# Kernel tuning notes

Measured on AMD Instinct MI355X. Metric: run time of the kernel, lower is better.

The kernel has to match this reference:

```python
import jax, jax.numpy as jnp
import numpy as np

N_NODES = 100000
N_EDGES = 3200000
IN_FEATS = 128
HIDDEN = 64
N_CLASSES = 16


def gcn_conv(x, src, dst, W, b, num_nodes):
    """PyG GCNConv (default settings): add self-loops, symmetric norm,
    linear transform, scatter-sum aggregation at dst, then bias."""
    # degree counts include self-loops (fill value 1.0)
    deg = jnp.zeros((num_nodes,), x.dtype).at[dst].add(1.0) + 1.0
    dinv = jax.lax.rsqrt(deg)  # deg >= 1, no inf handling needed
    h = x @ W  # [N, out]
    # edge messages: norm(src,dst) * h[src], aggregated at dst
    norm = dinv[src] * dinv[dst]  # [E]
    msg = h[src] * norm[:, None]  # [E, out]
    out = jax.ops.segment_sum(msg, dst, num_segments=num_nodes)
    # self-loop contribution: norm = dinv[i]^2
    out = out + h * (dinv * dinv)[:, None]
    return out + b


def setup_inputs() -> dict:
    key = jax.random.key(0)
    k1, k2, k3, k4 = jax.random.split(key, 4)
    x = jax.random.normal(k1, (N_NODES, IN_FEATS), dtype=jnp.float32)
    edge_index = jax.random.randint(k2, (2, N_EDGES), 0, N_NODES, dtype=jnp.int64)
    W1 = jax.random.normal(k3, (IN_FEATS, HIDDEN), dtype=jnp.float32) * (1.0 / np.sqrt(IN_FEATS))
    b1 = jnp.zeros((HIDDEN,), jnp.float32)
    W2 = jax.random.normal(k4, (HIDDEN, N_CLASSES), dtype=jnp.float32) * (1.0 / np.sqrt(HIDDEN))
    b2 = jnp.zeros((N_CLASSES,), jnp.float32)
    return {"x": x, "edge_index": edge_index, "W1": W1, "b1": b1, "W2": W2, "b2": b2}


def reference(x, edge_index, W1, b1, W2, b2):
    src, dst = edge_index[0], edge_index[1]
    h = gcn_conv(x, src, dst, W1, b1, N_NODES)
    h = jax.nn.relu(h)  # dropout is identity in eval mode
    out = gcn_conv(h, src, dst, W2, b2, N_NODES)
    return out
```

## Files before the change

### kernel.cpp

```cpp
#include <hip/hip_runtime.h>
#include <hip/hip_fp16.h>
#include <stdint.h>

#define N_NODES   100000
#define N_HALF    50000
#define N_EDGES   3200000
#define F_IN      128
#define F_HID     64
#define F_OUT     16

typedef _Float16 h2v __attribute__((ext_vector_type(2)));
typedef _Float16 h4v __attribute__((ext_vector_type(4)));

#define BSHIFT    8
#define NBUCK     391
#define NBLK_P    800
#define CHUNK_E   (N_EDGES / NBLK_P)
#define PSTRIDE   9856

#define G1_TM     128
#define G1_BLOCKS ((N_NODES + G1_TM - 1) / G1_TM)
#define XS_LD     132

#define OFF_RS       0
#define OFF_LEN      400000
#define OFF_DINV     800000
#define OFF_GCNT     1200000
#define OFF_CSR      1201616
#define OFF_HS1      8909008
#define OFF_OUT1A    21709008
#define OFF_OUT1B    34509008
#define OFF_HS2      47309008
#define OFF_PAIRS    OFF_OUT1A

__global__ __launch_bounds__(256, 4) void k_partition(const void* __restrict__ ei,
                                                      int* __restrict__ gcnt,
                                                      unsigned* __restrict__ pairs) {
    __shared__ unsigned long long st[CHUNK_E];
    __shared__ int h[NBUCK];
    __shared__ int cur[NBUCK];
    __shared__ int is64s;
    int t = threadIdx.x;
    if (t < 64) {
        const unsigned* u = (const unsigned*)ei;
        unsigned lo = u[2 * t], hi = u[2 * t + 1];
        int bad = (hi != 0u || lo >= 100000u) ? 1 : 0;
        unsigned long long mask = __ballot(bad);
        if (t == 0) is64s = (mask == 0ull);
    }
    for (int i = t; i < NBUCK; i += 256) h[i] = 0;
    __syncthreads();
    int shift = 2 + is64s;
    const char* sp = (const char*)ei;
    const char* dp = sp + ((size_t)N_EDGES << shift);
#define LDS_IDX(p, e) (*(const unsigned*)((p) + ((size_t)(e) << shift)))
    int base = blockIdx.x * CHUNK_E;
    int i = t;
    for (; i + 768 < CHUNK_E; i += 1024) {
        int e0 = base + i, e1 = e0 + 256, e2 = e0 + 512, e3 = e0 + 768;
        unsigned s0 = LDS_IDX(sp, e0), s1 = LDS_IDX(sp, e1);
        unsigned s2 = LDS_IDX(sp, e2), s3 = LDS_IDX(sp, e3);
        unsigned d0 = LDS_IDX(dp, e0), d1 = LDS_IDX(dp, e1);
        unsigned d2 = LDS_IDX(dp, e2), d3 = LDS_IDX(dp, e3);
        st[i]       = ((unsigned long long)s0 << 32) | d0;
        st[i + 256] = ((unsigned long long)s1 << 32) | d1;
        st[i + 512] = ((unsigned long long)s2 << 32) | d2;
        st[i + 768] = ((unsigned long long)s3 << 32) | d3;
        atomicAdd(&h[d0 >> BSHIFT], 1);
        atomicAdd(&h[d1 >> BSHIFT], 1);
        atomicAdd(&h[d2 >> BSHIFT], 1);
        atomicAdd(&h[d3 >> BSHIFT], 1);
    }
    for (; i < CHUNK_E; i += 256) {
        unsigned s = LDS_IDX(sp, base + i);
        unsigned d = LDS_IDX(dp, base + i);
        st[i] = ((unsigned long long)s << 32) | d;
        atomicAdd(&h[d >> BSHIFT], 1);
    }
#undef LDS_IDX
    __syncthreads();
    for (int j = t; j < NBUCK; j += 256) {
        int c = h[j];
        cur[j] = c ? atomicAdd(&gcnt[j], c) : 0;
    }
    __syncthreads();
    i = t;
    for (; i + 768 < CHUNK_E; i += 1024) {
        unsigned long long v0 = st[i],       v1 = st[i + 256];
        unsigned long long v2 = st[i + 512], v3 = st[i + 768];
        unsigned d0 = (unsigned)v0, d1 = (unsigned)v1;
        unsigned d2 = (unsigned)v2, d3 = (unsigned)v3;
        int p0 = atomicAdd(&cur[d0 >> BSHIFT], 1);
        int p1 = atomicAdd(&cur[d1 >> BSHIFT], 1);
        int p2 = atomicAdd(&cur[d2 >> BSHIFT], 1);
        int p3 = atomicAdd(&cur[d3 >> BSHIFT], 1);
        if (p0 < PSTRIDE) pairs[(d0 >> BSHIFT) * PSTRIDE + p0] = ((unsigned)(v0 >> 32) << 8) | (d0 & 255u);
        if (p1 < PSTRIDE) pairs[(d1 >> BSHIFT) * PSTRIDE + p1] = ((unsigned)(v1 >> 32) << 8) | (d1 & 255u);
        if (p2 < PSTRIDE) pairs[(d2 >> BSHIFT) * PSTRIDE + p2] = ((unsigned)(v2 >> 32) << 8) | (d2 & 255u);
        if (p3 < PSTRIDE) pairs[(d3 >> BSHIFT) * PSTRIDE + p3] = ((unsigned)(v3 >> 32) << 8) | (d3 & 255u);
    }
    for (; i < CHUNK_E; i += 256) {
        unsigned long long v = st[i];
        unsigned d = (unsigned)v;
        int b = d >> BSHIFT;
        int p = atomicAdd(&cur[b], 1);
        if (p < PSTRIDE)
            pairs[b * PSTRIDE + p] = ((unsigned)(v >> 32) << 8) | (d & 255u);
    }
}

__global__ __launch_bounds__(512) void k_build(const unsigned* __restrict__ pairs,
                                               const int* __restrict__ gcnt,
                                               int* __restrict__ rowstart,
                                               int* __restrict__ lens,
                                               float* __restrict__ dinv,
                                               unsigned short* __restrict__ csr) {
    __shared__ unsigned prS[PSTRIDE];
    __shared__ unsigned short csrS[PSTRIDE];
    __shared__ int c0S[256], c1S[256], scanS[256], pos0[256], pos1[256];
    __shared__ int totpadS;
    int b = blockIdx.x, t = threadIdx.x;
    if (t < 256) { c0S[t] = 0; c1S[t] = 0; }
    __syncthreads();
    int tot = gcnt[b]; if (tot > PSTRIDE) tot = PSTRIDE;
    int base = b * PSTRIDE;
    for (int i = t; i < tot; i += 512) {
        unsigned pr = pairs[base + i];
        prS[i] = pr;
        if ((pr >> 8) < (unsigned)N_HALF) atomicAdd(&c0S[pr & 255u], 1);
        else                              atomicAdd(&c1S[pr & 255u], 1);
    }
    __syncthreads();
    int tpad = 0, p0a = 0;
    if (t < 256) {
        p0a = (c0S[t] + 3) & ~3;
        tpad = p0a + ((c1S[t] + 3) & ~3);
        scanS[t] = tpad;
    }
    __syncthreads();
    for (int off = 1; off < 256; off <<= 1) {
        int add = 0;
        if (t < 256 && t >= off) add = scanS[t - off];
        __syncthreads();
        if (t < 256) scanS[t] += add;
        __syncthreads();
    }
    if (t < 256) {
        int rs = scanS[t] - tpad;
        pos0[t] = rs;
        pos1[t] = rs + p0a;
        int d = (b << BSHIFT) + t;
        if (d < N_NODES) {
            rowstart[d] = base + rs;
            lens[d] = c0S[t] | (c1S[t] << 16);
            dinv[d] = rsqrtf((float)(c0S[t] + c1S[t]) + 1.0f);
        }
        if (t == 255) totpadS = scanS[255];
    }
    __syncthreads();
    for (int i = t; i < tot; i += 512) {
        unsigned pr = prS[i];
        unsigned s = pr >> 8;
        int d = pr & 255u;
        if (s < (unsigned)N_HALF) {
            int p = atomicAdd(&pos0[d], 1);
            csrS[p] = (unsigned short)s;
        } else {
            int p = atomicAdd(&pos1[d], 1);
            csrS[p] = (unsigned short)(s - N_HALF);
        }
    }
    __syncthreads();
    int nchunk = (totpadS + 7) >> 3;
    uint4* dst = (uint4*)(csr + base);
    const uint4* srcp = (const uint4*)csrS;
    for (int i = t; i < nchunk; i += 512) dst[i] = srcp[i];
}

__global__ __launch_bounds__(256) void k_gemm1(const float* __restrict__ x,
                                               const float* __restrict__ W1,
                                               const float* __restrict__ dinv,
                                               __half* __restrict__ hs1) {
    __shared__ float xsT[64 * XS_LD];
    __shared__ float ws[64 * 64];
    int t = threadIdx.x;
    int nblock = blockIdx.x * G1_TM;
    int ng = t >> 4, og = t & 15;
    int n0 = ng * 8;
    float acc[8][4] = {};

    int snode = nblock + (t >> 1);
    int koff = (t & 1) * 32;
    int nl = t >> 1;

    for (int chunk = 0; chunk < 2; ++chunk) {
        int kbase = chunk * 64;
        {
            float4 v[8];
            if (snode < N_NODES) {
                const float4* src = (const float4*)(x + (size_t)snode * F_IN + kbase + koff);
#pragma unroll
                for (int c = 0; c < 8; ++c) v[c] = src[c];
            } else {
#pragma unroll
                for (int c = 0; c < 8; ++c) v[c] = make_float4(0.f, 0.f, 0.f, 0.f);
            }
#pragma unroll
            for (int c = 0; c < 8; ++c) {
                int k = koff + c * 4;
                xsT[(k + 0) * XS_LD + nl] = v[c].x;
                xsT[(k + 1) * XS_LD + nl] = v[c].y;
                xsT[(k + 2) * XS_LD + nl] = v[c].z;
                xsT[(k + 3) * XS_LD + nl] = v[c].w;
            }
        }
        {
            const float4* wsrc = (const float4*)(W1 + kbase * F_HID);
            float4* wdst = (float4*)ws;
#pragma unroll
            for (int c = 0; c < 4; ++c) wdst[c * 256 + t] = wsrc[c * 256 + t];
        }
        __syncthreads();

#pragma unroll 4
        for (int k = 0; k < 64; ++k) {
            const float4* xr = (const float4*)(xsT + k * XS_LD + n0);
            float4 a0 = xr[0], a1 = xr[1];
            float4 bv = *(const float4*)(ws + k * 64 + og * 4);
            float a[8] = {a0.x, a0.y, a0.z, a0.w, a1.x, a1.y, a1.z, a1.w};
            float bb[4] = {bv.x, bv.y, bv.z, bv.w};
#pragma unroll
            for (int i = 0; i < 8; ++i)
#pragma unroll
                for (int j = 0; j < 4; ++j)
                    acc[i][j] += a[i] * bb[j];
        }
        __syncthreads();
    }

#pragma unroll
    for (int i = 0; i < 8; ++i) {
        int node = nblock + n0 + i;
        if (node < N_NODES) {
            float dv = dinv[node];
            union { __half2 h[2]; float2 f; } u;
            u.h[0] = __floats2half2_rn(acc[i][0] * dv, acc[i][1] * dv);
            u.h[1] = __floats2half2_rn(acc[i][2] * dv, acc[i][3] * dv);
            *(float2*)(hs1 + ((size_t)(og >> 3) * N_NODES + node) * 32 + (og & 7) * 4) = u.f;
        }
    }
}

__global__ __launch_bounds__(256) void k_agg1(const __half* __restrict__ hs1,
                                              const unsigned short* __restrict__ csr,
                                              const int* __restrict__ rowstart,
                                              const int* __restrict__ lens,
                                              __half* __restrict__ out1a,
                                              __half* __restrict__ out1b) {
    int bid = blockIdx.x;
    int combo = bid & 3;
    int chunk = combo & 1, half = combo >> 1;
    int nb = bid >> 2;
    int w = threadIdx.x >> 6, lane = threadIdx.x & 63;
    int slot = lane >> 3, fp = lane & 7;
    int n = nb * 32 + w * 8 + slot;
    const char* T = (const char*)hs1
                  + (size_t)chunk * ((size_t)N_NODES * 64)
                  + (size_t)half * ((size_t)N_HALF * 64);
    unsigned fo = fp * 8u;
    int rs = rowstart[n];
    int L = lens[n];
    int c0 = L & 0xffff;
    int start = half ? (rs + ((c0 + 3) & ~3)) : rs;
    int c = half ? (L >> 16) : c0;
    h4v a0 = {(_Float16)0.f, (_Float16)0.f, (_Float16)0.f, (_Float16)0.f};
    h4v a1 = a0, a2 = a0, a3 = a0;
    const unsigned long long* Q = (const unsigned long long*)csr;
    int q0 = start >> 2;
    int nq = c >> 2;
#define ROW1(idx) (*(const h4v*)(T + (unsigned)(idx) * 64u + fo))
    int q = 0;
    unsigned long long ea = 0ull, eb = 0ull;
    if (q + 2 <= nq) { ea = Q[q0]; eb = Q[q0 + 1]; }
    while (q + 2 <= nq) {
        unsigned long long ca = ea, cb = eb;
        q += 2;
        if (q + 2 <= nq) { ea = Q[q0 + q]; eb = Q[q0 + q + 1]; }
        h4v t0 = ROW1(ca & 0xffffu);
        h4v t1 = ROW1((ca >> 16) & 0xffffu);
        h4v t2 = ROW1((ca >> 32) & 0xffffu);
        h4v t3 = ROW1(ca >> 48);
        h4v t4 = ROW1(cb & 0xffffu);
        h4v t5 = ROW1((cb >> 16) & 0xffffu);
        h4v t6 = ROW1((cb >> 32) & 0xffffu);
        h4v t7 = ROW1(cb >> 48);
        a0 += t0; a1 += t1; a2 += t2; a3 += t3;
        a0 += t4; a1 += t5; a2 += t6; a3 += t7;
    }
    if (q < nq) {
        unsigned long long e = Q[q0 + q];
        a0 += ROW1(e & 0xffffu);
        a1 += ROW1((e >> 16) & 0xffffu);
        a2 += ROW1((e >> 32) & 0xffffu);
        a3 += ROW1(e >> 48);
    }
    for (int j = start + (nq << 2); j < start + c; ++j)
        a0 += ROW1(csr[j]);
    if ((n >= N_HALF) == (half != 0))
        a1 += ROW1(n - half * N_HALF);
#undef ROW1
    float s0 = ((float)a0[0] + (float)a1[0]) + ((float)a2[0] + (float)a3[0]);
    float s1 = ((float)a0[1] + (float)a1[1]) + ((float)a2[1] + (float)a3[1]);
    float s2 = ((float)a0[2] + (float)a1[2]) + ((float)a2[2] + (float)a3[2]);
    float s3 = ((float)a0[3] + (float)a1[3]) + ((float)a2[3] + (float)a3[3]);
    union { __half2 h[2]; float2 f; } u;
    u.h[0] = __floats2half2_rn(s0, s1);
    u.h[1] = __floats2half2_rn(s2, s3);
    __half* dst = (half ? out1b : out1a) + (size_t)n * F_HID + chunk * 32 + fp * 4;
    *(float2*)dst = u.f;
}

__global__ __launch_bounds__(256) void k_gemm2(const __half* __restrict__ out1a,
                                               const __half* __restrict__ out1b,
                                               const float* __restrict__ W2,
                                               const float* __restrict__ dinv,
                                               const float* __restrict__ b1,
                                               __half* __restrict__ hs2) {
    __shared__ float ws[F_HID * F_OUT];
    __shared__ float b1s[F_HID];
    int t = threadIdx.x;
    ((float4*)ws)[t] = ((const float4*)W2)[t];
    if (t < 16) ((float4*)b1s)[t] = ((const float4*)b1)[t];
    __syncthreads();
    int tid = blockIdx.x * 256 + t;
    int n = tid >> 2;
    if (n >= N_NODES) return;
    int cq = (tid & 3) << 2;
    float dv = dinv[n];
    const h2v* A = (const h2v*)(out1a + (size_t)n * F_HID);
    const h2v* B = (const h2v*)(out1b + (size_t)n * F_HID);
    float4 acc = make_float4(0.f, 0.f, 0.f, 0.f);
#pragma unroll 4
    for (int k4 = 0; k4 < 16; ++k4) {
        h2v pa0 = A[k4 * 2], pa1 = A[k4 * 2 + 1];
        h2v pb0 = B[k4 * 2], pb1 = B[k4 * 2 + 1];
        float h0 = fmaxf(dv * ((float)pa0.x + (float)pb0.x) + b1s[k4 * 4 + 0], 0.f);
        float h1 = fmaxf(dv * ((float)pa0.y + (float)pb0.y) + b1s[k4 * 4 + 1], 0.f);
        float h2 = fmaxf(dv * ((float)pa1.x + (float)pb1.x) + b1s[k4 * 4 + 2], 0.f);
        float h3 = fmaxf(dv * ((float)pa1.y + (float)pb1.y) + b1s[k4 * 4 + 3], 0.f);
        float4 w0 = *(const float4*)(ws + (k4 * 4 + 0) * F_OUT + cq);
        float4 w1 = *(const float4*)(ws + (k4 * 4 + 1) * F_OUT + cq);
        float4 w2 = *(const float4*)(ws + (k4 * 4 + 2) * F_OUT + cq);
        float4 w3 = *(const float4*)(ws + (k4 * 4 + 3) * F_OUT + cq);
        acc.x += h0 * w0.x + h1 * w1.x + h2 * w2.x + h3 * w3.x;
        acc.y += h0 * w0.y + h1 * w1.y + h2 * w2.y + h3 * w3.y;
        acc.z += h0 * w0.z + h1 * w1.z + h2 * w2.z + h3 * w3.z;
        acc.w += h0 * w0.w + h1 * w1.w + h2 * w2.w + h3 * w3.w;
    }
    union { __half2 h2x[2]; float2 f; } u;
    u.h2x[0] = __floats2half2_rn(acc.x * dv, acc.y * dv);
    u.h2x[1] = __floats2half2_rn(acc.z * dv, acc.w * dv);
    *(float2*)(hs2 + (size_t)n * F_OUT + cq) = u.f;
}

__global__ __launch_bounds__(128) void k_agg2(const __half* __restrict__ hs2,
                                              const unsigned short* __restrict__ csr,
                                              const int* __restrict__ rowstart,
                                              const int* __restrict__ lens,
                                              const float* __restrict__ dinv,
                                              const float* __restrict__ b2,
                                              float* __restrict__ out) {
    int w = threadIdx.x >> 6, lane = threadIdx.x & 63;
    int slot = lane >> 2, fp = lane & 3;
    int n = blockIdx.x * 32 + w * 16 + slot;
    unsigned fo = fp * 8u;
    int rs = rowstart[n];
    int L = lens[n];
    int c0 = L & 0xffff, c1 = L >> 16;
    const unsigned long long* Q = (const unsigned long long*)csr;
    h4v a0 = {(_Float16)0.f, (_Float16)0.f, (_Float16)0.f, (_Float16)0.f};
    h4v a1 = a0, a2 = a0, a3 = a0;
#pragma unroll
    for (int half = 0; half < 2; ++half) {
        const char* T = (const char*)hs2 + (size_t)half * ((size_t)N_HALF * 32);
        int start = half ? (rs + ((c0 + 3) & ~3)) : rs;
        int c = half ? c1 : c0;
        int q0 = start >> 2;
        int nq = c >> 2;
#define ROW2(idx) (*(const h4v*)(T + (unsigned)(idx) * 32u + fo))
        int q = 0;
        unsigned long long ea = 0ull, eb = 0ull;
        if (q + 2 <= nq) { ea = Q[q0]; eb = Q[q0 + 1]; }
        while (q + 2 <= nq) {
            unsigned long long ca = ea, cb = eb;
            q += 2;
            if (q + 2 <= nq) { ea = Q[q0 + q]; eb = Q[q0 + q + 1]; }
            h4v t0 = ROW2(ca & 0xffffu);
            h4v t1 = ROW2((ca >> 16) & 0xffffu);
            h4v t2 = ROW2((ca >> 32) & 0xffffu);
            h4v t3 = ROW2(ca >> 48);
            h4v t4 = ROW2(cb & 0xffffu);
            h4v t5 = ROW2((cb >> 16) & 0xffffu);
            h4v t6 = ROW2((cb >> 32) & 0xffffu);
            h4v t7 = ROW2(cb >> 48);
            a0 += t0; a1 += t1; a2 += t2; a3 += t3;
            a0 += t4; a1 += t5; a2 += t6; a3 += t7;
        }
        if (q < nq) {
            unsigned long long e = Q[q0 + q];
            a0 += ROW2(e & 0xffffu);
            a1 += ROW2((e >> 16) & 0xffffu);
            a2 += ROW2((e >> 32) & 0xffffu);
            a3 += ROW2(e >> 48);
        }
        for (int j = start + (nq << 2); j < start + c; ++j)
            a0 += ROW2(csr[j]);
#undef ROW2
    }
    a1 += *(const h4v*)((const char*)hs2 + (unsigned)n * 32u + fo);
    float dv = dinv[n];
    int fb = fp * 4;
    float s0 = ((float)a0[0] + (float)a1[0]) + ((float)a2[0] + (float)a3[0]);
    float s1 = ((float)a0[1] + (float)a1[1]) + ((float)a2[1] + (float)a3[1]);
    float s2 = ((float)a0[2] + (float)a1[2]) + ((float)a2[2] + (float)a3[2]);
    float s3 = ((float)a0[3] + (float)a1[3]) + ((float)a2[3] + (float)a3[3]);
    float ox0 = dv * s0 + b2[fb + 0];
    float ox1 = dv * s1 + b2[fb + 1];
    float ox2 = dv * s2 + b2[fb + 2];
    float ox3 = dv * s3 + b2[fb + 3];
    float4* dst = (float4*)(out + (size_t)n * F_OUT + fb);
    *dst = make_float4(ox0, ox1, ox2, ox3);
}

extern "C" void kernel_launch(void* const* d_in, const int* in_sizes, int n_in,
                              void* d_out, int out_size, void* d_ws, size_t ws_size,
                              hipStream_t stream) {
    const float* x  = (const float*)d_in[0];
    const void*  ei = d_in[1];
    const float* W1 = (const float*)d_in[2];
    const float* b1 = (const float*)d_in[3];
    const float* W2 = (const float*)d_in[4];
    const float* b2 = (const float*)d_in[5];
    float* out = (float*)d_out;

    char* ws = (char*)d_ws;
    int*            rowstart = (int*)(ws + OFF_RS);
    int*            lens     = (int*)(ws + OFF_LEN);
    float*          dinv     = (float*)(ws + OFF_DINV);
    int*            gcnt     = (int*)(ws + OFF_GCNT);
    unsigned short* csr      = (unsigned short*)(ws + OFF_CSR);
    __half*         hs1      = (__half*)(ws + OFF_HS1);
    __half*         out1a    = (__half*)(ws + OFF_OUT1A);
    __half*         out1b    = (__half*)(ws + OFF_OUT1B);
    __half*         hs2      = (__half*)(ws + OFF_HS2);
    unsigned*       pairs    = (unsigned*)(ws + OFF_PAIRS);

    (void)hipMemsetAsync(gcnt, 0, NBUCK * sizeof(int), stream);
    k_partition<<<NBLK_P, 256, 0, stream>>>(ei, gcnt, pairs);
    k_build    <<<NBUCK, 512, 0, stream>>>(pairs, gcnt, rowstart, lens, dinv, csr);

    k_gemm1<<<G1_BLOCKS, 256, 0, stream>>>(x, W1, dinv, hs1);
    k_agg1 <<<12500, 256, 0, stream>>>(hs1, csr, rowstart, lens, out1a, out1b);
    k_gemm2<<<(N_NODES * 4 + 255) / 256, 256, 0, stream>>>(out1a, out1b, W2, dinv, b1, hs2);
    k_agg2 <<<3125, 128, 0, stream>>>(hs2, csr, rowstart, lens, dinv, b2, out);
}
```

Measured before the change: 281.4 us.

## Use nontemporal loads for streamed inputs and split agg1 into per-chunk launches

Streaming reads of edge indices, partition pairs and x in the gemm are switched to nontemporal loads so they do not evict reusable data from cache. The first aggregation kernel is split into two launches, one per 32-feature chunk of hs1, instead of interleaving both chunks across blocks in one launch. This shrinks the gather working set per launch (half the hs1 table) to improve L2 hit rate, at the cost of an extra launch and re-reading CSR indices twice serially.

Result: slower. 293.7 us (+4.4%).

```diff
diff --git a/kernel.cpp b/kernel.cpp
--- a/kernel.cpp
+++ b/kernel.cpp
@@ -11,6 +11,7 @@
 
 typedef _Float16 h2v __attribute__((ext_vector_type(2)));
 typedef _Float16 h4v __attribute__((ext_vector_type(4)));
+typedef float    f4v __attribute__((ext_vector_type(4)));
 
 #define BSHIFT    8
 #define NBUCK     391
@@ -53,7 +54,7 @@
     int shift = 2 + is64s;
     const char* sp = (const char*)ei;
     const char* dp = sp + ((size_t)N_EDGES << shift);
-#define LDS_IDX(p, e) (*(const unsigned*)((p) + ((size_t)(e) << shift)))
+#define LDS_IDX(p, e) __builtin_nontemporal_load((const unsigned*)((p) + ((size_t)(e) << shift)))
     int base = blockIdx.x * CHUNK_E;
     int i = t;
     for (; i + 768 < CHUNK_E; i += 1024) {
@@ -125,7 +126,7 @@
     int tot = gcnt[b]; if (tot > PSTRIDE) tot = PSTRIDE;
     int base = b * PSTRIDE;
     for (int i = t; i < tot; i += 512) {
-        unsigned pr = pairs[base + i];
+        unsigned pr = __builtin_nontemporal_load(pairs + base + i);
         prS[i] = pr;
         if ((pr >> 8) < (unsigned)N_HALF) atomicAdd(&c0S[pr & 255u], 1);
         else                              atomicAdd(&c1S[pr & 255u], 1);
@@ -196,22 +197,22 @@
     for (int chunk = 0; chunk < 2; ++chunk) {
         int kbase = chunk * 64;
         {
-            float4 v[8];
+            f4v v[8];
             if (snode < N_NODES) {
-                const float4* src = (const float4*)(x + (size_t)snode * F_IN + kbase + koff);
-#pragma unroll
-                for (int c = 0; c < 8; ++c) v[c] = src[c];
+                const f4v* src = (const f4v*)(x + (size_t)snode * F_IN + kbase + koff);
+#pragma unroll
+                for (int c = 0; c < 8; ++c) v[c] = __builtin_nontemporal_load(src + c);
             } else {
 #pragma unroll
-                for (int c = 0; c < 8; ++c) v[c] = make_float4(0.f, 0.f, 0.f, 0.f);
+                for (int c = 0; c < 8; ++c) v[c] = (f4v){0.f, 0.f, 0.f, 0.f};
             }
 #pragma unroll
             for (int c = 0; c < 8; ++c) {
                 int k = koff + c * 4;
-                xsT[(k + 0) * XS_LD + nl] = v[c].x;
-                xsT[(k + 1) * XS_LD + nl] = v[c].y;
-                xsT[(k + 2) * XS_LD + nl] = v[c].z;
-                xsT[(k + 3) * XS_LD + nl] = v[c].w;
+                xsT[(k + 0) * XS_LD + nl] = v[c][0];
+                xsT[(k + 1) * XS_LD + nl] = v[c][1];
+                xsT[(k + 2) * XS_LD + nl] = v[c][2];
+                xsT[(k + 3) * XS_LD + nl] = v[c][3];
             }
         }
         {
@@ -256,11 +257,11 @@
                                               const int* __restrict__ rowstart,
                                               const int* __restrict__ lens,
                                               __half* __restrict__ out1a,
-                                              __half* __restrict__ out1b) {
+                                              __half* __restrict__ out1b,
+                                              int chunk) {
     int bid = blockIdx.x;
-    int combo = bid & 3;
-    int chunk = combo & 1, half = combo >> 1;
-    int nb = bid >> 2;
+    int half = bid & 1;
+    int nb = bid >> 1;
     int w = threadIdx.x >> 6, lane = threadIdx.x & 63;
     int slot = lane >> 3, fp = lane & 7;
     int n = nb * 32 + w * 8 + slot;
@@ -460,7 +461,8 @@
     k_build    <<<NBUCK, 512, 0, stream>>>(pairs, gcnt, rowstart, lens, dinv, csr);
 
     k_gemm1<<<G1_BLOCKS, 256, 0, stream>>>(x, W1, dinv, hs1);
-    k_agg1 <<<12500, 256, 0, stream>>>(hs1, csr, rowstart, lens, out1a, out1b);
+    k_agg1 <<<6250, 256, 0, stream>>>(hs1, csr, rowstart, lens, out1a, out1b, 0);
+    k_agg1 <<<6250, 256, 0, stream>>>(hs1, csr, rowstart, lens, out1a, out1b, 1);
     k_gemm2<<<(N_NODES * 4 + 255) / 256, 256, 0, stream>>>(out1a, out1b, W2, dinv, b1, hs2);
     k_agg2 <<<3125, 128, 0, stream>>>(hs2, csr, rowstart, lens, dinv, b2, out);
 }
```

## Shrink gemm1 tiles for occupancy and use nontemporal loads for streamed inputs

Applied to the files above, without the earlier changes.

Halves the gemm1 node tile to 64 and the K chunk to 32, cuts per-thread accumulators from 8x4 to 4x4, and adds launch bounds requesting 4 blocks per CU. The aim is less LDS and fewer registers per block, so more blocks stay resident to hide the latency of streaming x. Edge-index, pairs and x reads now use nontemporal loads so these single-use streams do not evict cached data. In exchange W1 is reloaded per smaller block and there are more barrier rounds.

Result: no change. 282.9 us (+0.5%).

```diff
diff --git a/kernel.cpp b/kernel.cpp
--- a/kernel.cpp
+++ b/kernel.cpp
@@ -11,6 +11,7 @@
 
 typedef _Float16 h2v __attribute__((ext_vector_type(2)));
 typedef _Float16 h4v __attribute__((ext_vector_type(4)));
+typedef float    f4v __attribute__((ext_vector_type(4)));
 
 #define BSHIFT    8
 #define NBUCK     391
@@ -18,9 +19,9 @@
 #define CHUNK_E   (N_EDGES / NBLK_P)
 #define PSTRIDE   9856
 
-#define G1_TM     128
+#define G1_TM     64
 #define G1_BLOCKS ((N_NODES + G1_TM - 1) / G1_TM)
-#define XS_LD     132
+#define XS_LD     68
 
 #define OFF_RS       0
 #define OFF_LEN      400000
@@ -53,7 +54,7 @@
     int shift = 2 + is64s;
     const char* sp = (const char*)ei;
     const char* dp = sp + ((size_t)N_EDGES << shift);
-#define LDS_IDX(p, e) (*(const unsigned*)((p) + ((size_t)(e) << shift)))
+#define LDS_IDX(p, e) __builtin_nontemporal_load((const unsigned*)((p) + ((size_t)(e) << shift)))
     int base = blockIdx.x * CHUNK_E;
     int i = t;
     for (; i + 768 < CHUNK_E; i += 1024) {
@@ -125,7 +126,7 @@
     int tot = gcnt[b]; if (tot > PSTRIDE) tot = PSTRIDE;
     int base = b * PSTRIDE;
     for (int i = t; i < tot; i += 512) {
-        unsigned pr = pairs[base + i];
+        unsigned pr = __builtin_nontemporal_load(pairs + base + i);
         prS[i] = pr;
         if ((pr >> 8) < (unsigned)N_HALF) atomicAdd(&c0S[pr & 255u], 1);
         else                              atomicAdd(&c1S[pr & 255u], 1);
@@ -177,69 +178,65 @@
     for (int i = t; i < nchunk; i += 512) dst[i] = srcp[i];
 }
 
-__global__ __launch_bounds__(256) void k_gemm1(const float* __restrict__ x,
-                                               const float* __restrict__ W1,
-                                               const float* __restrict__ dinv,
-                                               __half* __restrict__ hs1) {
-    __shared__ float xsT[64 * XS_LD];
-    __shared__ float ws[64 * 64];
+__global__ __launch_bounds__(256, 4) void k_gemm1(const float* __restrict__ x,
+                                                  const float* __restrict__ W1,
+                                                  const float* __restrict__ dinv,
+                                                  __half* __restrict__ hs1) {
+    __shared__ float xsT[32 * XS_LD];
+    __shared__ float ws[32 * 64];
     int t = threadIdx.x;
     int nblock = blockIdx.x * G1_TM;
     int ng = t >> 4, og = t & 15;
-    int n0 = ng * 8;
-    float acc[8][4] = {};
-
-    int snode = nblock + (t >> 1);
-    int koff = (t & 1) * 32;
-    int nl = t >> 1;
-
-    for (int chunk = 0; chunk < 2; ++chunk) {
-        int kbase = chunk * 64;
+    int n0 = ng * 4;
+    float acc[4][4] = {};
+
+    int nl = t >> 2;
+    int koff = (t & 3) * 8;
+    int snode = nblock + nl;
+
+    for (int chunk = 0; chunk < 4; ++chunk) {
+        int kbase = chunk * 32;
         {
-            float4 v[8];
+            f4v v0, v1;
             if (snode < N_NODES) {
-                const float4* src = (const float4*)(x + (size_t)snode * F_IN + kbase + koff);
-#pragma unroll
-                for (int c = 0; c < 8; ++c) v[c] = src[c];
+                const f4v* src = (const f4v*)(x + (size_t)snode * F_IN + kbase + koff);
+                v0 = __builtin_nontemporal_load(src);
+                v1 = __builtin_nontemporal_load(src + 1);
             } else {
-#pragma unroll
-                for (int c = 0; c < 8; ++c) v[c] = make_float4(0.f, 0.f, 0.f, 0.f);
+                v0 = (f4v){0.f, 0.f, 0.f, 0.f};
+                v1 = v0;
             }
 #pragma unroll
-            for (int c = 0; c < 8; ++c) {
-                int k = koff + c * 4;
-                xsT[(k + 0) * XS_LD + nl] = v[c].x;
-                xsT[(k + 1) * XS_LD + nl] = v[c].y;
-                xsT[(k + 2) * XS_LD + nl] = v[c].z;
-                xsT[(k + 3) * XS_LD + nl] = v[c].w;
+            for (int i = 0; i < 4; ++i) {
+                xsT[(koff + i) * XS_LD + nl]     = v0[i];
+                xsT[(koff + 4 + i) * XS_LD + nl] = v1[i];
             }
         }
         {
             const float4* wsrc = (const float4*)(W1 + kbase * F_HID);
             float4* wdst = (float4*)ws;
-#pragma unroll
-            for (int c = 0; c < 4; ++c) wdst[c * 256 + t] = wsrc[c * 256 + t];
+            wdst[t]       = wsrc[t];
+            wdst[256 + t] = wsrc[256 + t];
         }
         __syncthreads();
 
-#pragma unroll 4
-        for (int k = 0; k < 64; ++k) {
-            const float4* xr = (const float4*)(xsT + k * XS_LD + n0);
-            float4 a0 = xr[0], a1 = xr[1];
+#pragma unroll 8
+        for (int k = 0; k < 32; ++k) {
+            float4 a = *(const float4*)(xsT + k * XS_LD + n0);
             float4 bv = *(const float4*)(ws + k * 64 + og * 4);
-            float a[8] = {a0.x, a0.y, a0.z, a0.w, a1.x, a1.y, a1.z, a1.w};
+            float aa[4] = {a.x, a.y, a.z, a.w};
             float bb[4] = {bv.x, bv.y, bv.z, bv.w};
 #pragma unroll
-            for (int i = 0; i < 8; ++i)
+            for (int i = 0; i < 4; ++i)
 #pragma unroll
                 for (int j = 0; j < 4; ++j)
-                    acc[i][j] += a[i] * bb[j];
+                    acc[i][j] += aa[i] * bb[j];
         }
         __syncthreads();
     }
 
 #pragma unroll
-    for (int i = 0; i < 8; ++i) {
+    for (int i = 0; i < 4; ++i) {
         int node = nblock + n0 + i;
         if (node < N_NODES) {
             float dv = dinv[node];
```
